# Optimization experiments

Measured on AMD Instinct MI355X. Metric: run time of the kernel, lower is better.

The kernel has to match this reference:

```python
import jax, jax.numpy as jnp
import numpy as np

NUM_CLASSES = 80
ALPHA = 0.25
GAMMA = 2.0
CONF_T = 0.5
IOU_T = 0.5
N_ANCHORS = 6144


def _pairwise_iou(b):
    # b: [n,4] (x1,y1,x2,y2) -> [n,n] IoU matrix
    area = (b[:, 2] - b[:, 0]) * (b[:, 3] - b[:, 1])
    lt = jnp.maximum(b[:, None, :2], b[None, :, :2])
    rb = jnp.minimum(b[:, None, 2:], b[None, :, 2:])
    wh = jnp.clip(rb - lt, 0.0)
    inter = wh[..., 0] * wh[..., 1]
    return inter / (area[:, None] + area[None, :] - inter)


def _nms(boxes, scores, thr):
    # torchvision-style NMS: returns kept indices in decreasing-score order
    order = jnp.argsort(-scores)
    iou = _pairwise_iou(boxes[order])
    n = boxes.shape[0]
    ar = jnp.arange(n)
    def body(i, supp):
        return supp | ((iou[i] > thr) & (ar > i) & jnp.logical_not(supp[i]))
    supp = jax.lax.fori_loop(0, n, body, jnp.zeros(n, dtype=bool))
    kept_pos = jnp.where(~supp)[0]  # eager: concrete shapes
    return order[kept_pos]


def _make_boxes(tb, floc):
    # tb: [1,1,4] target box; floc: [Nf,2] filtered predicted locations
    # replicates loc_determined with T=1: (tx1*px, ty1*py, tx2*px, ty2*py)
    px, py = floc[:, 0], floc[:, 1]
    return jnp.stack([tb[0, 0, 0] * px, tb[0, 0, 1] * py,
                      tb[0, 0, 2] * px, tb[0, 0, 3] * py], axis=1)


def _smooth_l1_sum(pred, tgt):
    d = jnp.abs(pred - tgt)  # broadcasts [k,C,4] vs [1,1,4]
    return jnp.where(d < 1.0, 0.5 * d * d, d - 0.5).sum()


def setup_inputs() -> dict:
    key = jax.random.key(0)
    k1, k2, k3 = jax.random.split(key, 3)
    locations = jax.random.uniform(k1, (1, N_ANCHORS, 2), dtype=jnp.float32)
    confidences = jax.random.uniform(k2, (1, N_ANCHORS, NUM_CLASSES), dtype=jnp.float32)
    # valid target box (x1<x2, y1<y2) in [0,1]
    target_boxes = jnp.array([[[0.15, 0.2, 0.85, 0.9]]], dtype=jnp.float32)
    target_labels = jax.random.randint(k3, (1,), 0, NUM_CLASSES)
    return {"locations": locations, "confidences": confidences,
            "target_boxes": target_boxes, "target_labels": target_labels}


def reference(locations, confidences, target_boxes, target_labels):
    conf = confidences[0]                       # [N,C]
    scores_max = conf.max(axis=1)
    idx_f = jnp.where(scores_max > CONF_T)[0]   # eager boolean filter
    if idx_f.shape[0] == 0:
        return jnp.float32(0.001)
    floc = locations[0, idx_f, :]               # [Nf,2]
    fconf = conf[idx_f]                         # [Nf,C]
    boxes = _make_boxes(target_boxes, floc)     # [Nf,4] (pred_loc_final)
    score = fconf[:, 0]                         # class-0 score, as in original
    keep = _nms(boxes, score, IOU_T)            # kept indices
    if keep.shape[0] == 0:
        return jnp.float32(0.001)
    matched_loc = boxes[keep]                   # [M,4]
    matched_conf = fconf[keep]                  # [M,C]
    k = target_labels.shape[0]                  # = 1
    topv, topi = jax.lax.top_k(matched_conf.T, k)  # per-class top-k over dim 0
    topv, topi = topv.T, topi.T                 # [k,C]
    pred_bin = (topv[:, 0] > 0.5).astype(jnp.float32)  # [k]
    mloc = matched_loc[topi]                    # [k,C,4]
    loc_loss = _smooth_l1_sum(mloc, target_boxes)
    # F.cross_entropy with 1-D float input/target = probabilities mode, unbatched
    ce = -(target_labels.astype(jnp.float32) * jax.nn.log_softmax(pred_bin)).sum()
    focal = ALPHA * (1.0 - jnp.exp(-ce)) ** GAMMA * ce
    # original bug preserved: num_positives = sum of kept *indices*
    num_pos = keep.sum().astype(jnp.float32)
    return (loc_loss + focal) / num_pos
```

## Files before the change

### kernel.cpp

```cpp
#include <hip/hip_runtime.h>
#include <stdint.h>

#define N_ANCHORS 6144
#define NUM_CLASSES 80
#define NWORDS 96

__device__ unsigned long long g_mask[(size_t)N_ANCHORS * NWORDS];
__device__ float4 g_boxes[N_ANCHORS];
__device__ float4 g_sbox[N_ANCHORS];
__device__ float  g_key[N_ANCHORS];
__device__ int    g_rank[N_ANCHORS];
__device__ int    g_fic[N_ANCHORS];
__device__ int    g_sAnchor[N_ANCHORS];
__device__ int    g_sFi[N_ANCHORS];
__device__ int    g_keptPos[N_ANCHORS];
__device__ int    g_F, g_K, g_np, g_done;
__device__ float  g_loss;

__device__ __forceinline__ unsigned long long shfl64(unsigned long long v, int l) {
    return __shfl(v, l, 64);
}

__global__ void k_prep(const float* __restrict__ loc, const float* __restrict__ conf,
                       const float* __restrict__ tb) {
    int i = blockIdx.x * 256 + threadIdx.x;
    if (i >= N_ANCHORS) return;
    g_rank[i] = 0; g_fic[i] = 0;
    if (i == 0) { g_F = 0; g_K = 0; g_np = 0; g_loss = 0.0f; g_done = 0; }
    const float4* cp4 = (const float4*)(conf + (size_t)i * NUM_CLASSES);
    float4 v0 = cp4[0];
    float score = v0.x;
    float m = fmaxf(fmaxf(v0.x, v0.y), fmaxf(v0.z, v0.w));
    #pragma unroll
    for (int c = 1; c < NUM_CLASSES / 4; ++c) {
        float4 v = cp4[c];
        m = fmaxf(m, fmaxf(fmaxf(v.x, v.y), fmaxf(v.z, v.w)));
    }
    bool valid = m > 0.5f;
    g_key[i] = valid ? score : -1.0f;
    float px = loc[2 * i], py = loc[2 * i + 1];
    float4 b;
    b.x = __fmul_rn(tb[0], px);
    b.y = __fmul_rn(tb[1], py);
    b.z = __fmul_rn(tb[2], px);
    b.w = __fmul_rn(tb[3], py);
    g_boxes[i] = b;
}

__global__ void k_rank(void) {
    __shared__ float skey[256];
    int j0 = blockIdx.y * 256;
    skey[threadIdx.x] = g_key[j0 + threadIdx.x];
    __syncthreads();
    int i = blockIdx.x * 256 + threadIdx.x;
    float ki = g_key[i];
    int r = 0, f = 0;
    #pragma unroll 8
    for (int jj = 0; jj < 256; ++jj) {
        float kj = skey[jj];
        int j = j0 + jj;
        bool valid_j = kj >= 0.0f;
        r += (kj > ki) || (kj == ki && j < i && valid_j);
        f += (j < i) && valid_j;
    }
    atomicAdd(&g_rank[i], r);
    atomicAdd(&g_fic[i], f);
}

__global__ void k_scatter(void) {
    int i = blockIdx.x * 256 + threadIdx.x;
    if (i >= N_ANCHORS) return;
    if (g_key[i] >= 0.0f) {
        int p = g_rank[i];
        g_sAnchor[p] = i;
        g_sFi[p] = g_fic[i];
        g_sbox[p] = g_boxes[i];
        atomicAdd(&g_F, 1);
    }
}

__global__ void __launch_bounds__(256) k_mask(void) {
    int wave = (blockIdx.x * 256 + threadIdx.x) >> 6;
    int lane = threadIdx.x & 63;
    if (wave >= N_ANCHORS) return;
    int i = wave;
    float4 bi = g_sbox[i];
    float areai = __fmul_rn(bi.z - bi.x, bi.w - bi.y);
    unsigned long long* row = g_mask + (size_t)i * NWORDS;
    for (int w = (i >> 6); w < NWORDS; ++w) {
        float4 bj = g_sbox[w * 64 + lane];
        float areaj = __fmul_rn(bj.z - bj.x, bj.w - bj.y);
        float lx = fmaxf(bi.x, bj.x), ly = fmaxf(bi.y, bj.y);
        float rx = fminf(bi.z, bj.z), ry = fminf(bi.w, bj.w);
        float iw = fmaxf(rx - lx, 0.0f), ih = fmaxf(ry - ly, 0.0f);
        float inter = __fmul_rn(iw, ih);
        float denom = __fsub_rn(__fadd_rn(areai, areaj), inter);
        float iou = __fdiv_rn(inter, denom);
        unsigned long long bits = __ballot(iou > 0.5f);
        if (lane == 0) row[w] = bits;
    }
}

#define SCAN_B 16
__global__ void __launch_bounds__(64) k_scan(void) {
    int lane = threadIdx.x;
    int F = g_F;
    auto initw = [&](int w) -> unsigned long long {
        long long lo = (long long)w * 64, hi = lo + 64;
        if (F <= lo) return ~0ull;
        if (F >= hi) return 0ull;
        return (~0ull) << (F - lo);
    };
    unsigned long long remv0 = initw(lane);
    unsigned long long remv1 = (lane < 32) ? initw(64 + lane) : ~0ull;
    unsigned long long kept0 = 0, kept1 = 0;
    int lastPos = -1;

    __shared__ int slots[SCAN_B];

    while (true) {
        unsigned long long c0 = ~remv0;
        unsigned long long c1 = (lane < 32) ? ~remv1 : 0ull;
        {
            long long lo = (long long)lane << 6;
            if (lastPos >= lo + 63)      c0 = 0ull;
            else if (lastPos >= lo)      c0 &= (~0ull) << (int)(lastPos - lo + 1);
        }
        if (lane < 32) {
            long long lo = (long long)(64 + lane) << 6;
            if (lastPos >= lo + 63)      c1 = 0ull;
            else if (lastPos >= lo)      c1 &= (~0ull) << (int)(lastPos - lo + 1);
        }
        int n0 = __popcll(c0), n1 = __popcll(c1);
        int x0 = n0, x1 = n1;
        for (int ofs = 1; ofs < 64; ofs <<= 1) {
            int y0 = __shfl_up(x0, ofs, 64);
            int y1 = __shfl_up(x1, ofs, 64);
            if (lane >= ofs) { x0 += y0; x1 += y1; }
        }
        int tot0 = __shfl(x0, 63, 64);
        int tot1 = __shfl(x1, 63, 64);
        int total = tot0 + tot1;
        if (total == 0) break;
        int off0 = x0 - n0;
        int off1 = tot0 + (x1 - n1);
        {
            unsigned long long wd = c0; int r = off0;
            while (wd && r < SCAN_B) { int b = __builtin_ctzll(wd); slots[r++] = lane * 64 + b; wd &= wd - 1; }
        }
        if (lane < 32) {
            unsigned long long wd = c1; int r = off1;
            while (wd && r < SCAN_B) { int b = __builtin_ctzll(wd); slots[r++] = (64 + lane) * 64 + b; wd &= wd - 1; }
        }
        __syncthreads();
        int nb = (total < SCAN_B) ? total : SCAN_B;
        int pos[SCAN_B];
        #pragma unroll
        for (int q = 0; q < SCAN_B; ++q) pos[q] = (q < nb) ? slots[q] : -1;
        __syncthreads();

        unsigned long long r0[SCAN_B], r1[SCAN_B];
        #pragma unroll
        for (int q = 0; q < SCAN_B; ++q) {
            if (pos[q] >= 0) {
                const unsigned long long* rp = g_mask + (size_t)pos[q] * NWORDS;
                r0[q] = rp[lane];
                r1[q] = (lane < 32) ? rp[64 + lane] : 0ull;
            } else { r0[q] = 0ull; r1[q] = 0ull; }
        }

        #pragma unroll
        for (int q = 0; q < SCAN_B; ++q) {
            if (pos[q] >= 0) {
                int w = pos[q] >> 6, b = pos[q] & 63;
                unsigned long long cw = (w < 64) ? shfl64(remv0, w) : shfl64(remv1, w - 64);
                if (!((cw >> b) & 1ull)) {
                    remv0 |= r0[q];
                    if (lane < 32) remv1 |= r1[q];
                    if (w < 64) { if (lane == w) kept0 |= 1ull << b; }
                    else        { if (lane == w - 64) kept1 |= 1ull << b; }
                }
                lastPos = pos[q];
            }
        }
    }

    int c0 = __popcll(kept0);
    int c1 = (lane < 32) ? __popcll(kept1) : 0;
    int x0 = c0, x1 = c1;
    for (int ofs = 1; ofs < 64; ofs <<= 1) {
        int y0 = __shfl_up(x0, ofs, 64);
        int y1 = __shfl_up(x1, ofs, 64);
        if (lane >= ofs) { x0 += y0; x1 += y1; }
    }
    int t0 = __shfl(x0, 63, 64);
    int t1 = __shfl(x1, 63, 64);
    int off = x0 - c0;
    unsigned long long wd = kept0;
    while (wd) { int b = __builtin_ctzll(wd); g_keptPos[off++] = lane * 64 + b; wd &= wd - 1; }
    off = t0 + (x1 - c1);
    wd = kept1;
    while (wd) { int b = __builtin_ctzll(wd); g_keptPos[off++] = (64 + lane) * 64 + b; wd &= wd - 1; }
    if (lane == 0) g_K = t0 + t1;
}

__global__ void __launch_bounds__(64) k_loss(const float* __restrict__ conf, const float* __restrict__ tb,
                                             float* __restrict__ out) {
    int c = blockIdx.x;
    int lane = threadIdx.x;
    int K = g_K;
    float bv = -3.402823466e+38f;
    int bk = 0x7fffffff;
    int np = 0;
    for (int k = lane; k < K; k += 64) {
        int p = g_keptPos[k];
        int a = g_sAnchor[p];
        float v = conf[(size_t)a * NUM_CLASSES + c];
        if (v > bv || (v == bv && k < bk)) { bv = v; bk = k; }
        if (c == 0) np += g_sFi[p];
    }
    for (int ofs = 32; ofs > 0; ofs >>= 1) {
        float ov = __shfl_down(bv, ofs, 64);
        int ok = __shfl_down(bk, ofs, 64);
        if (ov > bv || (ov == bv && ok < bk)) { bv = ov; bk = ok; }
    }
    if (c == 0) {
        for (int ofs = 32; ofs > 0; ofs >>= 1) np += __shfl_down(np, ofs, 64);
        if (lane == 0) atomicExch(&g_np, np);
    }
    if (lane == 0) {
        if (K > 0) {
            float4 b = g_sbox[g_keptPos[bk]];
            float t0 = tb[0], t1 = tb[1], t2 = tb[2], t3 = tb[3];
            float l = 0.0f, d;
            d = fabsf(b.x - t0); l += (d < 1.0f) ? 0.5f * d * d : d - 0.5f;
            d = fabsf(b.y - t1); l += (d < 1.0f) ? 0.5f * d * d : d - 0.5f;
            d = fabsf(b.z - t2); l += (d < 1.0f) ? 0.5f * d * d : d - 0.5f;
            d = fabsf(b.w - t3); l += (d < 1.0f) ? 0.5f * d * d : d - 0.5f;
            atomicAdd(&g_loss, l);
        }
        __threadfence();
        int done = atomicAdd(&g_done, 1);
        if (done == NUM_CLASSES - 1) {
            float total = atomicAdd(&g_loss, 0.0f);
            int npv = atomicAdd(&g_np, 0);
            out[0] = (g_F == 0 || K == 0) ? 0.001f : total / (float)npv;
        }
    }
}

extern "C" void kernel_launch(void* const* d_in, const int* in_sizes, int n_in,
                              void* d_out, int out_size, void* d_ws, size_t ws_size,
                              hipStream_t stream) {
    const float* loc  = (const float*)d_in[0];
    const float* conf = (const float*)d_in[1];
    const float* tb   = (const float*)d_in[2];
    float* out = (float*)d_out;

    k_prep<<<24, 256, 0, stream>>>(loc, conf, tb);
    k_rank<<<dim3(24, 24), 256, 0, stream>>>();
    k_scatter<<<24, 256, 0, stream>>>();
    k_mask<<<(N_ANCHORS * 64) / 256, 256, 0, stream>>>();
    k_scan<<<1, 64, 0, stream>>>();
    k_loss<<<NUM_CLASSES, 64, 0, stream>>>(conf, tb, out);
}
```

Before: 159.1 us.

## Fuse prep into rank and scatter, replace atomics with partial-sum arrays

Removes the separate prep kernel by recomputing the per-anchor key from the confidences inside the rank and scatter kernels, and computes boxes only in scatter. Rank partial counts are written to per-tile arrays and summed in scatter instead of being accumulated with atomics, which also removes the need to zero counters. F is derived from the last anchor's prefix count rather than an atomic counter, and the loss accumulators are reset in the scan kernel. The scan batch size doubles. In exchange, the 80-float confidence row is re-read in every rank tile, adding redundant global loads.

```diff
diff --git a/kernel.cpp b/kernel.cpp
--- a/kernel.cpp
+++ b/kernel.cpp
@@ -4,13 +4,12 @@
 #define N_ANCHORS 6144
 #define NUM_CLASSES 80
 #define NWORDS 96
+#define NTILES 24
 
 __device__ unsigned long long g_mask[(size_t)N_ANCHORS * NWORDS];
-__device__ float4 g_boxes[N_ANCHORS];
 __device__ float4 g_sbox[N_ANCHORS];
-__device__ float  g_key[N_ANCHORS];
-__device__ int    g_rank[N_ANCHORS];
-__device__ int    g_fic[N_ANCHORS];
+__device__ int    g_rpart[NTILES][N_ANCHORS];
+__device__ int    g_fpart[NTILES][N_ANCHORS];
 __device__ int    g_sAnchor[N_ANCHORS];
 __device__ int    g_sFi[N_ANCHORS];
 __device__ int    g_keptPos[N_ANCHORS];
@@ -21,12 +20,7 @@
     return __shfl(v, l, 64);
 }
 
-__global__ void k_prep(const float* __restrict__ loc, const float* __restrict__ conf,
-                       const float* __restrict__ tb) {
-    int i = blockIdx.x * 256 + threadIdx.x;
-    if (i >= N_ANCHORS) return;
-    g_rank[i] = 0; g_fic[i] = 0;
-    if (i == 0) { g_F = 0; g_K = 0; g_np = 0; g_loss = 0.0f; g_done = 0; }
+__device__ __forceinline__ float anchor_key(const float* __restrict__ conf, int i, bool& valid) {
     const float4* cp4 = (const float4*)(conf + (size_t)i * NUM_CLASSES);
     float4 v0 = cp4[0];
     float score = v0.x;
@@ -36,24 +30,20 @@
         float4 v = cp4[c];
         m = fmaxf(m, fmaxf(fmaxf(v.x, v.y), fmaxf(v.z, v.w)));
     }
-    bool valid = m > 0.5f;
-    g_key[i] = valid ? score : -1.0f;
-    float px = loc[2 * i], py = loc[2 * i + 1];
-    float4 b;
-    b.x = __fmul_rn(tb[0], px);
-    b.y = __fmul_rn(tb[1], py);
-    b.z = __fmul_rn(tb[2], px);
-    b.w = __fmul_rn(tb[3], py);
-    g_boxes[i] = b;
-}
-
-__global__ void k_rank(void) {
+    valid = m > 0.5f;
+    return valid ? score : -1.0f;
+}
+
+__global__ void __launch_bounds__(256) k_rank(const float* __restrict__ conf) {
     __shared__ float skey[256];
-    int j0 = blockIdx.y * 256;
-    skey[threadIdx.x] = g_key[j0 + threadIdx.x];
+    int y = blockIdx.y;
+    int j0 = y * 256;
+    bool vj;
+    skey[threadIdx.x] = anchor_key(conf, j0 + threadIdx.x, vj);
+    int i = blockIdx.x * 256 + threadIdx.x;
+    bool vi;
+    float ki = anchor_key(conf, i, vi);
     __syncthreads();
-    int i = blockIdx.x * 256 + threadIdx.x;
-    float ki = g_key[i];
     int r = 0, f = 0;
     #pragma unroll 8
     for (int jj = 0; jj < 256; ++jj) {
@@ -63,20 +53,32 @@
         r += (kj > ki) || (kj == ki && j < i && valid_j);
         f += (j < i) && valid_j;
     }
-    atomicAdd(&g_rank[i], r);
-    atomicAdd(&g_fic[i], f);
-}
-
-__global__ void k_scatter(void) {
+    g_rpart[y][i] = r;
+    g_fpart[y][i] = f;
+}
+
+__global__ void __launch_bounds__(256) k_scatter(const float* __restrict__ loc,
+                                                 const float* __restrict__ conf,
+                                                 const float* __restrict__ tb) {
     int i = blockIdx.x * 256 + threadIdx.x;
-    if (i >= N_ANCHORS) return;
-    if (g_key[i] >= 0.0f) {
-        int p = g_rank[i];
-        g_sAnchor[p] = i;
-        g_sFi[p] = g_fic[i];
-        g_sbox[p] = g_boxes[i];
-        atomicAdd(&g_F, 1);
-    }
+    bool vi;
+    float ki = anchor_key(conf, i, vi);
+    (void)ki;
+    int r = 0, f = 0;
+    #pragma unroll
+    for (int y = 0; y < NTILES; ++y) { r += g_rpart[y][i]; f += g_fpart[y][i]; }
+    if (vi) {
+        float px = loc[2 * i], py = loc[2 * i + 1];
+        float4 b;
+        b.x = __fmul_rn(tb[0], px);
+        b.y = __fmul_rn(tb[1], py);
+        b.z = __fmul_rn(tb[2], px);
+        b.w = __fmul_rn(tb[3], py);
+        g_sbox[r] = b;
+        g_sAnchor[r] = i;
+        g_sFi[r] = f;
+    }
+    if (i == N_ANCHORS - 1) g_F = f + (vi ? 1 : 0);
 }
 
 __global__ void __launch_bounds__(256) k_mask(void) {
@@ -101,10 +103,11 @@
     }
 }
 
-#define SCAN_B 16
-__global__ void __launch_bounds__(64) k_scan(void) {
+#define SCAN_B 32
+__global__ void __launch_bounds__(64, 1) k_scan(void) {
     int lane = threadIdx.x;
     int F = g_F;
+    if (lane == 0) { g_loss = 0.0f; g_np = 0; g_done = 0; }
     auto initw = [&](int w) -> unsigned long long {
         long long lo = (long long)w * 64, hi = lo + 64;
         if (F <= lo) return ~0ull;
@@ -257,9 +260,8 @@
     const float* tb   = (const float*)d_in[2];
     float* out = (float*)d_out;
 
-    k_prep<<<24, 256, 0, stream>>>(loc, conf, tb);
-    k_rank<<<dim3(24, 24), 256, 0, stream>>>();
-    k_scatter<<<24, 256, 0, stream>>>();
+    k_rank<<<dim3(NTILES, NTILES), 256, 0, stream>>>(conf);
+    k_scatter<<<NTILES, 256, 0, stream>>>(loc, conf, tb);
     k_mask<<<(N_ANCHORS * 64) / 256, 256, 0, stream>>>();
     k_scan<<<1, 64, 0, stream>>>();
     k_loss<<<NUM_CLASSES, 64, 0, stream>>>(conf, tb, out);
```

After: 164.8 us. 1.04x slower.
